# Kernel optimization log

Hardware: AMD Instinct MI355X
Metric: run time of the kernel (lower is better)

## Reference

```python
import jax, jax.numpy as jnp
import numpy as np

D = 128
N_DATA = 100000
N_TASK = 20000
E = 1000000


def _conv_params(key, d):
    ks = jax.random.split(key, 9)
    s = 1.0 / np.sqrt(d)
    return dict(
        Wmn=jax.random.uniform(ks[0], (d, d), jnp.float32, -s, s),
        bmn=jnp.zeros((d,), jnp.float32),
        Wme=jax.random.uniform(ks[1], (d, 1), jnp.float32, -1.0, 1.0),
        bme=jnp.zeros((d,), jnp.float32),
        Wgn=jax.random.uniform(ks[2], (d, d), jnp.float32, -s, s),
        bgn=jnp.zeros((d,), jnp.float32),
        Wge=jax.random.uniform(ks[3], (d, 1), jnp.float32, -1.0, 1.0),
        bge=jnp.zeros((d,), jnp.float32),
        bias=jnp.zeros((d,), jnp.float32),  # HeteConvLayer bias, zeros-init
    )


def setup_inputs() -> dict:
    key = jax.random.key(0)
    ks = jax.random.split(key, 12)
    inp = {
        'x_data': jax.random.normal(ks[0], (N_DATA, D), jnp.float32),
        'x_task': jax.random.normal(ks[1], (N_TASK, D), jnp.float32),
        'src_dt': jax.random.randint(ks[2], (E,), 0, N_DATA, jnp.int32),
        'dst_dt': jax.random.randint(ks[3], (E,), 0, N_TASK, jnp.int32),
        'ef_dt': jax.random.uniform(ks[4], (E, 1), jnp.float32),
        'src_td': jax.random.randint(ks[5], (E,), 0, N_TASK, jnp.int32),
        'dst_td': jax.random.randint(ks[6], (E,), 0, N_DATA, jnp.int32),
        'ef_td': jax.random.uniform(ks[7], (E, 1), jnp.float32),
    }
    # two separate HeteConvLayers (cfg.kg.hete=True)
    for name, k in (('dt', ks[8]), ('td', ks[9])):
        for pn, pv in _conv_params(k, D).items():
            inp[pn + '_' + name] = pv
    s = 1.0 / np.sqrt(D)
    inp['Ws_data'] = jax.random.uniform(ks[10], (D, D), jnp.float32, -s, s)
    inp['bs_data'] = jnp.zeros((D,), jnp.float32)
    inp['Ws_task'] = jax.random.uniform(ks[11], (D, D), jnp.float32, -s, s)
    inp['bs_task'] = jnp.zeros((D,), jnp.float32)
    return inp


def _hete_conv(x_neigh, src, dst, ef, Wmn, bmn, Wme, bme, Wgn, bgn, Wge, bge, bias, n_out):
    xj = x_neigh[src]                                   # [E, D] gather
    msg = xj @ Wmn.T + bmn + ef @ Wme.T + bme           # [E, D]
    gate = jax.nn.sigmoid(xj @ Wgn.T + bgn + ef @ Wge.T + bge) - 0.5  # gate_bias
    msg = msg * gate
    return jax.ops.segment_sum(msg, dst, num_segments=n_out) + bias


def _self_layer(x, Ws, bs):
    return (jax.nn.sigmoid(x @ Ws.T + bs) + 0.5) * x    # SelfLayer, gate_bias=True


def reference(x_data, x_task, src_dt, dst_dt, ef_dt, src_td, dst_td, ef_td,
              Wmn_dt, bmn_dt, Wme_dt, bme_dt, Wgn_dt, bgn_dt, Wge_dt, bge_dt, bias_dt,
              Wmn_td, bmn_td, Wme_td, bme_td, Wgn_td, bgn_td, Wge_td, bge_td, bias_td,
              Ws_data, bs_data, Ws_task, bs_task):
    # message type (data, property, task): neigh=data, self=task
    agg_task = _hete_conv(x_data, src_dt, dst_dt, ef_dt,
                          Wmn_dt, bmn_dt, Wme_dt, bme_dt,
                          Wgn_dt, bgn_dt, Wge_dt, bge_dt, bias_dt, N_TASK)
    # message type (task, property, data): neigh=task, self=data
    agg_data = _hete_conv(x_task, src_td, dst_td, ef_td,
                          Wmn_td, bmn_td, Wme_td, bme_td,
                          Wgn_td, bgn_td, Wge_td, bge_td, bias_td, N_DATA)
    # add self-transform, aggr='add', then Postlayer = ReLU
    data_emb = jax.nn.relu(agg_data + _self_layer(x_data, Ws_data, bs_data))
    task_emb = jax.nn.relu(agg_task + _self_layer(x_task, Ws_task, bs_task))
    # concatenate node-type outputs along node axis for a single output array
    return jnp.concatenate([data_emb, task_emb], axis=0)
```

## Files before the change

kernel.cpp:

```cpp
#include <hip/hip_runtime.h>
#include <hip/hip_bf16.h>
#include <cstdint>
#include <cstddef>

#define D_DIM 128
#define NEG_LOG2E (-1.44269504f)

typedef __attribute__((ext_vector_type(8))) short short8;
typedef __attribute__((ext_vector_type(4))) float f32x4;

__device__ __forceinline__ float sigmoid_fast(float z) {
  return __builtin_amdgcn_rcpf(1.0f + __expf(-z));
}

__device__ __forceinline__ unsigned short f2bf(float f) {
  union { float f; unsigned u; } v; v.f = f;
  unsigned r = v.u + 0x7FFF + ((v.u >> 16) & 1);
  return (unsigned short)(r >> 16);
}
__device__ __forceinline__ float bf_lo(unsigned u) { return __uint_as_float(u << 16); }
__device__ __forceinline__ float bf_hi(unsigned u) { return __uint_as_float(u & 0xFFFF0000u); }

__global__ __launch_bounds__(256) void fused_pre_kernel(
    const float* __restrict__ s0, const float* __restrict__ s1, const float* __restrict__ s2,
    const float* __restrict__ s3, const float* __restrict__ s4, const float* __restrict__ s5,
    short* __restrict__ wdst,
    const int* __restrict__ dst_dt, const int* __restrict__ dst_td,
    int* __restrict__ ghist, int* __restrict__ done,
    int* __restrict__ bbase, int* __restrict__ bcur, int* __restrict__ offsets,
    int nbt, int NB, int E, int n_tot) {
  __shared__ int lh[768];
  __shared__ int sc[256];
  __shared__ int lastflag;
  int t = threadIdx.x;

  if (blockIdx.x < 96) {
    int idx = blockIdx.x * 256 + t;
    int mat = idx >> 12;
    int pos = (idx & 4095) * 4;
    const float* s = (mat == 0) ? s0 : (mat == 1) ? s1 : (mat == 2) ? s2
                   : (mat == 3) ? s3 : (mat == 4) ? s4 : s5;
    float4 f = *(const float4*)(s + pos);
    short4 o;
    o.x = (short)f2bf(f.x); o.y = (short)f2bf(f.y);
    o.z = (short)f2bf(f.z); o.w = (short)f2bf(f.w);
    *(short4*)(wdst + mat * 16384 + pos) = o;
  }

  lh[t] = 0; lh[t + 256] = 0; lh[t + 512] = 0;
  __syncthreads();
  int E4 = E >> 2;
  for (int i = blockIdx.x * 256 + t; i < E4; i += gridDim.x * 256) {
    int4 a = *(const int4*)(dst_dt + 4 * i);
    atomicAdd(&lh[a.x >> 6], 1); atomicAdd(&lh[a.y >> 6], 1);
    atomicAdd(&lh[a.z >> 6], 1); atomicAdd(&lh[a.w >> 6], 1);
    int4 b = *(const int4*)(dst_td + 4 * i);
    atomicAdd(&lh[nbt + (b.x >> 8)], 1); atomicAdd(&lh[nbt + (b.y >> 8)], 1);
    atomicAdd(&lh[nbt + (b.z >> 8)], 1); atomicAdd(&lh[nbt + (b.w >> 8)], 1);
  }
  if (blockIdx.x == 0 && t < (E & 3)) {
    int j = (E & ~3) + t;
    atomicAdd(&lh[dst_dt[j] >> 6], 1);
    atomicAdd(&lh[nbt + (dst_td[j] >> 8)], 1);
  }
  __syncthreads();
#pragma unroll
  for (int k = 0; k < 3; ++k) {
    int b = t + k * 256;
    int c = lh[b];
    if (b < NB && c) atomicAdd(&ghist[b], c);
  }
  __threadfence();
  __syncthreads();
  if (t == 0) {
    int prev = atomicAdd(done, 1);
    lastflag = (prev == (int)gridDim.x - 1);
  }
  __syncthreads();
  if (!lastflag) return;
  __threadfence();

  int i0 = t * 3;
  int c0 = (i0     < NB) ? atomicAdd(&ghist[i0],     0) : 0;
  int c1 = (i0 + 1 < NB) ? atomicAdd(&ghist[i0 + 1], 0) : 0;
  int c2 = (i0 + 2 < NB) ? atomicAdd(&ghist[i0 + 2], 0) : 0;
  int tot = c0 + c1 + c2;
  sc[t] = tot; __syncthreads();
  for (int s = 1; s < 256; s <<= 1) {
    int u = (t >= s) ? sc[t - s] : 0;
    __syncthreads(); sc[t] += u; __syncthreads();
  }
  int base = sc[t] - tot;
  if (i0     < NB) { bbase[i0]     = base;           bcur[i0]     = base; }
  if (i0 + 1 < NB) { bbase[i0 + 1] = base + c0;      bcur[i0 + 1] = base + c0; }
  if (i0 + 2 < NB) { bbase[i0 + 2] = base + c0 + c1; bcur[i0 + 2] = base + c0 + c1; }
  if (t == 255) { bbase[NB] = sc[255]; offsets[n_tot] = sc[255]; }
}

__global__ __launch_bounds__(256) void node_mfma_all(
    const float* __restrict__ x_data, const float* __restrict__ x_task,
    const short* __restrict__ Wb,
    const float* __restrict__ bmn_dt, const float* __restrict__ bme_dt,
    const float* __restrict__ bgn_dt, const float* __restrict__ bge_dt,
    const float* __restrict__ bmn_td, const float* __restrict__ bme_td,
    const float* __restrict__ bgn_td, const float* __restrict__ bge_td,
    const float* __restrict__ bs_data, const float* __restrict__ bs_task,
    const float* __restrict__ bias_dt, const float* __restrict__ bias_td,
    unsigned int* __restrict__ YG_dt, unsigned int* __restrict__ YG_td,
    float* __restrict__ out, int n_data, int n_task, int gd) {
  __shared__ unsigned sh[32][132];
  const bool is_data = (int)blockIdx.x < gd;
  const float* x; const short *Wmnb, *Wgnb, *Wsb;
  const float *bmn, *bme, *bgn, *bge, *bs, *bias_other;
  unsigned* YG; float* out_init; int n, bid;
  if (is_data) {
    x = x_data; Wmnb = Wb; Wgnb = Wb + 16384; Wsb = Wb + 32768;
    bmn = bmn_dt; bme = bme_dt; bgn = bgn_dt; bge = bge_dt;
    bs = bs_data; bias_other = bias_td;
    YG = YG_dt; out_init = out; n = n_data; bid = blockIdx.x;
  } else {
    x = x_task; Wmnb = Wb + 3 * 16384; Wgnb = Wb + 4 * 16384; Wsb = Wb + 5 * 16384;
    bmn = bmn_td; bme = bme_td; bgn = bgn_td; bge = bge_td;
    bs = bs_task; bias_other = bias_dt;
    YG = YG_td; out_init = out + (size_t)n_data * D_DIM; n = n_task; bid = blockIdx.x - gd;
  }
  const int t = threadIdx.x;
  const int wave = t >> 6, lane = t & 63;
  const int q = lane >> 4, l15 = lane & 15;
  const int ng = wave >> 1;
  const int h = (wave & 1) * 64;
  const int base_node = bid * 32;
  const int node_base = base_node + ng * 16;

  short8 a[4];
  {
    int m = node_base + l15;
    int mc = m < n ? m : (n - 1);
    const float* xrow = x + (size_t)mc * D_DIM;
#pragma unroll
    for (int ks = 0; ks < 4; ++ks) {
      float4 f0 = *(const float4*)(xrow + ks * 32 + q * 8);
      float4 f1 = *(const float4*)(xrow + ks * 32 + q * 8 + 4);
      union { short8 s; __hip_bfloat162 hh[4]; } u;
      u.hh[0] = __float22bfloat162_rn({f0.x, f0.y});
      u.hh[1] = __float22bfloat162_rn({f0.z, f0.w});
      u.hh[2] = __float22bfloat162_rn({f1.x, f1.y});
      u.hh[3] = __float22bfloat162_rn({f1.z, f1.w});
      a[ks] = u.s;
    }
  }

  f32x4 accY[4], accG[4], accS[4];
#pragma unroll
  for (int nt = 0; nt < 4; ++nt) { accY[nt] = {0,0,0,0}; accG[nt] = {0,0,0,0}; accS[nt] = {0,0,0,0}; }

#pragma unroll
  for (int nt = 0; nt < 4; ++nt) {
    const int row = h + nt * 16 + l15;
#pragma unroll
    for (int ks = 0; ks < 4; ++ks) {
      const int off = row * D_DIM + ks * 32 + q * 8;
      short8 bm  = *(const short8*)(Wmnb + off);
      short8 bg  = *(const short8*)(Wgnb + off);
      short8 bsw = *(const short8*)(Wsb + off);
      accY[nt] = __builtin_amdgcn_mfma_f32_16x16x32_bf16(a[ks], bm,  accY[nt], 0, 0, 0);
      accG[nt] = __builtin_amdgcn_mfma_f32_16x16x32_bf16(a[ks], bg,  accG[nt], 0, 0, 0);
      accS[nt] = __builtin_amdgcn_mfma_f32_16x16x32_bf16(a[ks], bsw, accS[nt], 0, 0, 0);
    }
  }

#pragma unroll
  for (int nt = 0; nt < 4; ++nt) {
    int d = h + nt * 16 + l15;
    float bmv = bmn[d] + bme[d];
    float bgv = bgn[d] + bge[d];
#pragma unroll
    for (int r = 0; r < 4; ++r) {
      union { __hip_bfloat162 hh; unsigned u; } pck;
      pck.hh = __float22bfloat162_rn({accY[nt][r] + bmv,
                                      (accG[nt][r] + bgv) * NEG_LOG2E});
      sh[ng * 16 + q * 4 + r][d] = pck.u;
    }
  }
  __syncthreads();
#pragma unroll
  for (int it = 0; it < 4; ++it) {
    int idx = (it * 256 + t) * 4;
    int nl = idx >> 7, dd = idx & 127;
    int node = base_node + nl;
    if (node < n)
      *(uint4*)(YG + (size_t)node * D_DIM + dd) = *(const uint4*)&sh[nl][dd];
  }
  __syncthreads();

  float* shf = (float*)sh;
#pragma unroll
  for (int nt = 0; nt < 4; ++nt) {
    int d = h + nt * 16 + l15;
    float bsv = bs[d];
#pragma unroll
    for (int r = 0; r < 4; ++r)
      shf[(ng * 16 + q * 4 + r) * 132 + d] = sigmoid_fast(accS[nt][r] + bsv) + 0.5f;
  }
  __syncthreads();
#pragma unroll
  for (int it = 0; it < 4; ++it) {
    int idx = (it * 256 + t) * 4;
    int nl = idx >> 7, dd = idx & 127;
    int node = base_node + nl;
    if (node < n) {
      float4 xv = *(const float4*)(x + (size_t)node * D_DIM + dd);
      float4 bo = *(const float4*)(bias_other + dd);
      const float* sp = &shf[nl * 132 + dd];
      float4 o;
      o.x = sp[0] * xv.x + bo.x;
      o.y = sp[1] * xv.y + bo.y;
      o.z = sp[2] * xv.z + bo.z;
      o.w = sp[3] * xv.w + bo.w;
      *(float4*)(out_init + (size_t)node * D_DIM + dd) = o;
    }
  }
}

__global__ __launch_bounds__(256) void sort_a_kernel(
    const int* __restrict__ src_dt, const int* __restrict__ dst_dt, const float* __restrict__ ef_dt,
    const int* __restrict__ src_td, const int* __restrict__ dst_td, const float* __restrict__ ef_td,
    int* __restrict__ bcur, int2* __restrict__ eA, int nbt, int NB, int E) {
  __shared__ int lh[768];
  __shared__ int lcur[768];
  int t = threadIdx.x;
  lh[t] = 0; lh[t + 256] = 0; lh[t + 512] = 0;
  __syncthreads();
  int e0 = blockIdx.x * 4096;
  int e1 = min(E, e0 + 4096);
  const bool full = (e1 - e0 == 4096);
  if (full) {
#pragma unroll
    for (int k = 0; k < 4; ++k) {
      int b4 = e0 + (k * 256 + t) * 4;
      int4 d = *(const int4*)(dst_dt + b4);
      atomicAdd(&lh[d.x >> 6], 1); atomicAdd(&lh[d.y >> 6], 1);
      atomicAdd(&lh[d.z >> 6], 1); atomicAdd(&lh[d.w >> 6], 1);
      int4 d2 = *(const int4*)(dst_td + b4);
      atomicAdd(&lh[nbt + (d2.x >> 8)], 1); atomicAdd(&lh[nbt + (d2.y >> 8)], 1);
      atomicAdd(&lh[nbt + (d2.z >> 8)], 1); atomicAdd(&lh[nbt + (d2.w >> 8)], 1);
    }
  } else {
    for (int i = e0 + t; i < e1; i += 256) {
      atomicAdd(&lh[dst_dt[i] >> 6], 1);
      atomicAdd(&lh[nbt + (dst_td[i] >> 8)], 1);
    }
  }
  __syncthreads();
#pragma unroll
  for (int k = 0; k < 3; ++k) {
    int b = t + k * 256;
    int c = lh[b];
    if (b < NB && c) lcur[b] = atomicAdd(&bcur[b], c);
  }
  __syncthreads();
#define PUT_DT(ss, dd, ff) do { \
    int pos = atomicAdd(&lcur[(dd) >> 6], 1); \
    eA[pos] = make_int2((ss), (int)((__float_as_uint(ff) & 0xFFFFFF00u) | (unsigned)((dd) & 63))); \
  } while (0)
#define PUT_TD(ss, dd, ff) do { \
    int pos = atomicAdd(&lcur[nbt + ((dd) >> 8)], 1); \
    eA[pos] = make_int2((ss), (int)((__float_as_uint(ff) & 0xFFFFFF00u) | (unsigned)((dd) & 255))); \
  } while (0)
  if (full) {
#pragma unroll
    for (int k = 0; k < 4; ++k) {
      int b4 = e0 + (k * 256 + t) * 4;
      int4 s = *(const int4*)(src_dt + b4);
      int4 d = *(const int4*)(dst_dt + b4);
      float4 f = *(const float4*)(ef_dt + b4);
      PUT_DT(s.x, d.x, f.x); PUT_DT(s.y, d.y, f.y);
      PUT_DT(s.z, d.z, f.z); PUT_DT(s.w, d.w, f.w);
      s = *(const int4*)(src_td + b4);
      d = *(const int4*)(dst_td + b4);
      f = *(const float4*)(ef_td + b4);
      PUT_TD(s.x, d.x, f.x); PUT_TD(s.y, d.y, f.y);
      PUT_TD(s.z, d.z, f.z); PUT_TD(s.w, d.w, f.w);
    }
  } else {
    for (int i = e0 + t; i < e1; i += 256) {
      PUT_DT(src_dt[i], dst_dt[i], ef_dt[i]);
      PUT_TD(src_td[i], dst_td[i], ef_td[i]);
    }
  }
#undef PUT_DT
#undef PUT_TD
}

__global__ __launch_bounds__(256) void sort_b_kernel(
    const int2* __restrict__ eA, const int* __restrict__ bbase,
    int* __restrict__ offsets, int2* __restrict__ eB,
    int nbt, int n_task, int n_tot) {
  __shared__ int lh[256], sc[256], lcur[256];
  int b = blockIdx.x, t = threadIdx.x;
  int base = bbase[b];
  int cnt = bbase[b + 1] - base;
  int c0, nloc;
  if (b < nbt) { c0 = b << 6; nloc = min(64, n_task - c0); }
  else { c0 = n_task + ((b - nbt) << 8); nloc = min(256, n_tot - c0); }
  lh[t] = 0; __syncthreads();
  for (int i = base + t; i < base + cnt; i += 256)
    atomicAdd(&lh[((unsigned)eA[i].y) & 255u], 1);
  __syncthreads();
  int v = lh[t];
  sc[t] = v; __syncthreads();
  for (int s = 1; s < 256; s <<= 1) {
    int u = (t >= s) ? sc[t - s] : 0;
    __syncthreads(); sc[t] += u; __syncthreads();
  }
  int ex = sc[t] - v;
  lcur[t] = base + ex;
  if (t < nloc) offsets[c0 + t] = base + ex;
  __syncthreads();
  for (int i = base + t; i < base + cnt; i += 256) {
    int2 e = eA[i];
    int pos = atomicAdd(&lcur[((unsigned)e.y) & 255u], 1);
    eB[pos] = e;
  }
}

__device__ __forceinline__ void gs(float2& acc, int2 e, uint2 yv,
                                   float2 wme, float2 wge2) {
  float f = __int_as_float(e.y & (int)0xFFFFFF00);
  float g0 = __builtin_amdgcn_rcpf(1.0f + __builtin_amdgcn_exp2f(fmaf(f, wge2.x, bf_hi(yv.x)))) - 0.5f;
  float g1 = __builtin_amdgcn_rcpf(1.0f + __builtin_amdgcn_exp2f(fmaf(f, wge2.y, bf_hi(yv.y)))) - 0.5f;
  acc.x = fmaf(fmaf(f, wme.x, bf_lo(yv.x)), g0, acc.x);
  acc.y = fmaf(fmaf(f, wme.y, bf_lo(yv.y)), g1, acc.y);
}

__global__ __launch_bounds__(256) void gather_kernel(
    const unsigned* __restrict__ YG_dt, const unsigned* __restrict__ YG_td,
    const int* __restrict__ offsets, const int2* __restrict__ edata,
    const float* __restrict__ Wme_dt, const float* __restrict__ Wge_dt,
    const float* __restrict__ Wme_td, const float* __restrict__ Wge_td,
    float* __restrict__ out, int n_task, int n_data) {
  int w = (int)((blockIdx.x * 256u + threadIdx.x) >> 6);
  int lane = threadIdx.x & 63;
  if (w >= n_task + n_data) return;
  bool is_dt = w < n_task;
  const unsigned* YG = is_dt ? YG_dt : YG_td;
  const float* Wme = is_dt ? Wme_dt : Wme_td;
  const float* Wge = is_dt ? Wge_dt : Wge_td;
  size_t orow = is_dt ? (size_t)(n_data + w) : (size_t)(w - n_task);
  int beg = __builtin_amdgcn_readfirstlane(offsets[w]);
  int end = __builtin_amdgcn_readfirstlane(offsets[w + 1]);
  float2 wme = *(const float2*)(Wme + 2 * lane);
  float2 wge = *(const float2*)(Wge + 2 * lane);
  float2 wge2 = {wge.x * NEG_LOG2E, wge.y * NEG_LOG2E};
  float* op = out + orow * D_DIM + 2 * lane;
  float2 acc0 = *(const float2*)op;
  float2 acc1 = {0.0f, 0.0f}, acc2 = {0.0f, 0.0f}, acc3 = {0.0f, 0.0f};
  int p = beg;
#define YGLD(e) (*(const uint2*)(YG + (size_t)(e).x * D_DIM + 2 * lane))
  if (p + 8 <= end) {
    int2 e0 = edata[p],     e1 = edata[p + 1], e2 = edata[p + 2], e3 = edata[p + 3];
    int2 e4 = edata[p + 4], e5 = edata[p + 5], e6 = edata[p + 6], e7 = edata[p + 7];
    uint2 y0 = YGLD(e0), y1 = YGLD(e1), y2 = YGLD(e2), y3 = YGLD(e3);
    uint2 y4 = YGLD(e4), y5 = YGLD(e5), y6 = YGLD(e6), y7 = YGLD(e7);
    p += 8;
    for (; p + 8 <= end; p += 8) {
      int2 f0 = edata[p],     f1 = edata[p + 1], f2 = edata[p + 2], f3 = edata[p + 3];
      int2 f4 = edata[p + 4], f5 = edata[p + 5], f6 = edata[p + 6], f7 = edata[p + 7];
      uint2 z0 = YGLD(f0), z1 = YGLD(f1), z2 = YGLD(f2), z3 = YGLD(f3);
      uint2 z4 = YGLD(f4), z5 = YGLD(f5), z6 = YGLD(f6), z7 = YGLD(f7);
      gs(acc0, e0, y0, wme, wge2); gs(acc1, e1, y1, wme, wge2);
      gs(acc2, e2, y2, wme, wge2); gs(acc3, e3, y3, wme, wge2);
      gs(acc0, e4, y4, wme, wge2); gs(acc1, e5, y5, wme, wge2);
      gs(acc2, e6, y6, wme, wge2); gs(acc3, e7, y7, wme, wge2);
      e0 = f0; e1 = f1; e2 = f2; e3 = f3; e4 = f4; e5 = f5; e6 = f6; e7 = f7;
      y0 = z0; y1 = z1; y2 = z2; y3 = z3; y4 = z4; y5 = z5; y6 = z6; y7 = z7;
    }
    gs(acc0, e0, y0, wme, wge2); gs(acc1, e1, y1, wme, wge2);
    gs(acc2, e2, y2, wme, wge2); gs(acc3, e3, y3, wme, wge2);
    gs(acc0, e4, y4, wme, wge2); gs(acc1, e5, y5, wme, wge2);
    gs(acc2, e6, y6, wme, wge2); gs(acc3, e7, y7, wme, wge2);
  }
  for (; p < end; ++p) {
    int2 et = edata[p];
    uint2 yt = YGLD(et);
    gs(acc0, et, yt, wme, wge2);
  }
#undef YGLD
  acc0.x = fmaxf(acc0.x + acc1.x + acc2.x + acc3.x, 0.0f);
  acc0.y = fmaxf(acc0.y + acc1.y + acc2.y + acc3.y, 0.0f);
  *(float2*)op = acc0;
}

extern "C" void kernel_launch(void* const* d_in, const int* in_sizes, int n_in,
                              void* d_out, int out_size, void* d_ws, size_t ws_size,
                              hipStream_t stream) {
  const float* x_data  = (const float*)d_in[0];
  const float* x_task  = (const float*)d_in[1];
  const int*   src_dt  = (const int*)d_in[2];
  const int*   dst_dt  = (const int*)d_in[3];
  const float* ef_dt   = (const float*)d_in[4];
  const int*   src_td  = (const int*)d_in[5];
  const int*   dst_td  = (const int*)d_in[6];
  const float* ef_td   = (const float*)d_in[7];
  const float* Wmn_dt  = (const float*)d_in[8];
  const float* bmn_dt  = (const float*)d_in[9];
  const float* Wme_dt  = (const float*)d_in[10];
  const float* bme_dt  = (const float*)d_in[11];
  const float* Wgn_dt  = (const float*)d_in[12];
  const float* bgn_dt  = (const float*)d_in[13];
  const float* Wge_dt  = (const float*)d_in[14];
  const float* bge_dt  = (const float*)d_in[15];
  const float* bias_dt = (const float*)d_in[16];
  const float* Wmn_td  = (const float*)d_in[17];
  const float* bmn_td  = (const float*)d_in[18];
  const float* Wme_td  = (const float*)d_in[19];
  const float* bme_td  = (const float*)d_in[20];
  const float* Wgn_td  = (const float*)d_in[21];
  const float* bgn_td  = (const float*)d_in[22];
  const float* Wge_td  = (const float*)d_in[23];
  const float* bge_td  = (const float*)d_in[24];
  const float* bias_td = (const float*)d_in[25];
  const float* Ws_data = (const float*)d_in[26];
  const float* bs_data = (const float*)d_in[27];
  const float* Ws_task = (const float*)d_in[28];
  const float* bs_task = (const float*)d_in[29];
  float* out = (float*)d_out;

  const int N_DATA = in_sizes[0] / D_DIM;
  const int N_TASK = in_sizes[1] / D_DIM;
  const int E = in_sizes[2];
  const int N_TOT = N_TASK + N_DATA;
  const int NBT = (N_TASK + 63) >> 6;
  const int NBD = (N_DATA + 255) >> 8;
  const int NB = NBT + NBD;
  const int GD = (N_DATA + 31) / 32;
  const int GT = (N_TASK + 31) / 32;

  char* ws = (char*)d_ws;
  size_t off = 0;
  auto alloc = [&](size_t bytes) { void* p = ws + off; off += (bytes + 255) & ~(size_t)255; return p; };
  unsigned int* YG_dt = (unsigned int*)alloc((size_t)N_DATA * D_DIM * 4);
  unsigned int* YG_td = (unsigned int*)alloc((size_t)N_TASK * D_DIM * 4);
  int2* eA     = (int2*)alloc((size_t)2 * E * 8);
  int2* eB     = (int2*)alloc((size_t)2 * E * 8);
  int*  offs   = (int*)alloc((size_t)(N_TOT + 1) * 4);
  int*  ghist  = (int*)alloc(1024 * 4);
  int*  bbase  = (int*)alloc(768 * 4);
  int*  bcur   = (int*)alloc(768 * 4);
  short* Wb    = (short*)alloc((size_t)6 * 16384 * 2);
  (void)ws_size; (void)n_in; (void)out_size;

  hipMemsetAsync(ghist, 0, 1024 * 4, stream);

  fused_pre_kernel<<<256, 256, 0, stream>>>(
      Wmn_dt, Wgn_dt, Ws_data, Wmn_td, Wgn_td, Ws_task, Wb,
      dst_dt, dst_td, ghist, ghist + 768, bbase, bcur, offs,
      NBT, NB, E, N_TOT);

  node_mfma_all<<<GD + GT, 256, 0, stream>>>(
      x_data, x_task, Wb,
      bmn_dt, bme_dt, bgn_dt, bge_dt,
      bmn_td, bme_td, bgn_td, bge_td,
      bs_data, bs_task, bias_dt, bias_td,
      YG_dt, YG_td, out, N_DATA, N_TASK, GD);

  sort_a_kernel<<<(E + 4095) / 4096, 256, 0, stream>>>(
      src_dt, dst_dt, ef_dt, src_td, dst_td, ef_td, bcur, eA, NBT, NB, E);
  sort_b_kernel<<<NB, 256, 0, stream>>>(eA, bbase, offs, eB, NBT, N_TASK, N_TOT);

  gather_kernel<<<(N_TOT + 3) / 4, 256, 0, stream>>>(
      YG_dt, YG_td, offs, eB, Wme_dt, Wge_dt, Wme_td, Wge_td, out, N_TASK, N_DATA);
}
```

Baseline: 477.1 us.

## Split gather into per-relation launches, pre-scale source indices, drop software pipelining

```diff
diff --git a/kernel.cpp b/kernel.cpp
--- a/kernel.cpp
+++ b/kernel.cpp
@@ -320,7 +320,7 @@
   for (int i = base + t; i < base + cnt; i += 256) {
     int2 e = eA[i];
     int pos = atomicAdd(&lcur[((unsigned)e.y) & 255u], 1);
-    eB[pos] = e;
+    eB[pos] = make_int2(e.x << 7, e.y);
   }
 }
 
@@ -333,61 +333,47 @@
   acc.y = fmaf(fmaf(f, wme.y, bf_lo(yv.y)), g1, acc.y);
 }
 
-__global__ __launch_bounds__(256) void gather_kernel(
-    const unsigned* __restrict__ YG_dt, const unsigned* __restrict__ YG_td,
+__global__ __launch_bounds__(256) void gather_one_kernel(
+    const unsigned* __restrict__ YG,
     const int* __restrict__ offsets, const int2* __restrict__ edata,
-    const float* __restrict__ Wme_dt, const float* __restrict__ Wge_dt,
-    const float* __restrict__ Wme_td, const float* __restrict__ Wge_td,
-    float* __restrict__ out, int n_task, int n_data) {
+    const float* __restrict__ Wme, const float* __restrict__ Wge,
+    float* __restrict__ outp, int n) {
   int w = (int)((blockIdx.x * 256u + threadIdx.x) >> 6);
   int lane = threadIdx.x & 63;
-  if (w >= n_task + n_data) return;
-  bool is_dt = w < n_task;
-  const unsigned* YG = is_dt ? YG_dt : YG_td;
-  const float* Wme = is_dt ? Wme_dt : Wme_td;
-  const float* Wge = is_dt ? Wge_dt : Wge_td;
-  size_t orow = is_dt ? (size_t)(n_data + w) : (size_t)(w - n_task);
+  if (w >= n) return;
   int beg = __builtin_amdgcn_readfirstlane(offsets[w]);
   int end = __builtin_amdgcn_readfirstlane(offsets[w + 1]);
   float2 wme = *(const float2*)(Wme + 2 * lane);
   float2 wge = *(const float2*)(Wge + 2 * lane);
   float2 wge2 = {wge.x * NEG_LOG2E, wge.y * NEG_LOG2E};
-  float* op = out + orow * D_DIM + 2 * lane;
+  const unsigned* YGl = YG + 2 * lane;
+  float* op = outp + (size_t)w * D_DIM + 2 * lane;
   float2 acc0 = *(const float2*)op;
-  float2 acc1 = {0.0f, 0.0f}, acc2 = {0.0f, 0.0f}, acc3 = {0.0f, 0.0f};
+  float2 acc1 = {0.0f, 0.0f};
   int p = beg;
-#define YGLD(e) (*(const uint2*)(YG + (size_t)(e).x * D_DIM + 2 * lane))
-  if (p + 8 <= end) {
+  for (; p + 8 <= end; p += 8) {
     int2 e0 = edata[p],     e1 = edata[p + 1], e2 = edata[p + 2], e3 = edata[p + 3];
     int2 e4 = edata[p + 4], e5 = edata[p + 5], e6 = edata[p + 6], e7 = edata[p + 7];
-    uint2 y0 = YGLD(e0), y1 = YGLD(e1), y2 = YGLD(e2), y3 = YGLD(e3);
-    uint2 y4 = YGLD(e4), y5 = YGLD(e5), y6 = YGLD(e6), y7 = YGLD(e7);
-    p += 8;
-    for (; p + 8 <= end; p += 8) {
-      int2 f0 = edata[p],     f1 = edata[p + 1], f2 = edata[p + 2], f3 = edata[p + 3];
-      int2 f4 = edata[p + 4], f5 = edata[p + 5], f6 = edata[p + 6], f7 = edata[p + 7];
-      uint2 z0 = YGLD(f0), z1 = YGLD(f1), z2 = YGLD(f2), z3 = YGLD(f3);
-      uint2 z4 = YGLD(f4), z5 = YGLD(f5), z6 = YGLD(f6), z7 = YGLD(f7);
-      gs(acc0, e0, y0, wme, wge2); gs(acc1, e1, y1, wme, wge2);
-      gs(acc2, e2, y2, wme, wge2); gs(acc3, e3, y3, wme, wge2);
-      gs(acc0, e4, y4, wme, wge2); gs(acc1, e5, y5, wme, wge2);
-      gs(acc2, e6, y6, wme, wge2); gs(acc3, e7, y7, wme, wge2);
-      e0 = f0; e1 = f1; e2 = f2; e3 = f3; e4 = f4; e5 = f5; e6 = f6; e7 = f7;
-      y0 = z0; y1 = z1; y2 = z2; y3 = z3; y4 = z4; y5 = z5; y6 = z6; y7 = z7;
-    }
-    gs(acc0, e0, y0, wme, wge2); gs(acc1, e1, y1, wme, wge2);
-    gs(acc2, e2, y2, wme, wge2); gs(acc3, e3, y3, wme, wge2);
-    gs(acc0, e4, y4, wme, wge2); gs(acc1, e5, y5, wme, wge2);
-    gs(acc2, e6, y6, wme, wge2); gs(acc3, e7, y7, wme, wge2);
-  }
-  for (; p < end; ++p) {
-    int2 et = edata[p];
-    uint2 yt = YGLD(et);
-    gs(acc0, et, yt, wme, wge2);
-  }
-#undef YGLD
-  acc0.x = fmaxf(acc0.x + acc1.x + acc2.x + acc3.x, 0.0f);
-  acc0.y = fmaxf(acc0.y + acc1.y + acc2.y + acc3.y, 0.0f);
+    gs(acc0, e0, *(const uint2*)(YGl + e0.x), wme, wge2);
+    gs(acc1, e1, *(const uint2*)(YGl + e1.x), wme, wge2);
+    gs(acc0, e2, *(const uint2*)(YGl + e2.x), wme, wge2);
+    gs(acc1, e3, *(const uint2*)(YGl + e3.x), wme, wge2);
+    gs(acc0, e4, *(const uint2*)(YGl + e4.x), wme, wge2);
+    gs(acc1, e5, *(const uint2*)(YGl + e5.x), wme, wge2);
+    gs(acc0, e6, *(const uint2*)(YGl + e6.x), wme, wge2);
+    gs(acc1, e7, *(const uint2*)(YGl + e7.x), wme, wge2);
+  }
+  for (; p + 2 <= end; p += 2) {
+    int2 e0 = edata[p], e1 = edata[p + 1];
+    gs(acc0, e0, *(const uint2*)(YGl + e0.x), wme, wge2);
+    gs(acc1, e1, *(const uint2*)(YGl + e1.x), wme, wge2);
+  }
+  if (p < end) {
+    int2 e0 = edata[p];
+    gs(acc0, e0, *(const uint2*)(YGl + e0.x), wme, wge2);
+  }
+  acc0.x = fmaxf(acc0.x + acc1.x, 0.0f);
+  acc0.y = fmaxf(acc0.y + acc1.y, 0.0f);
   *(float2*)op = acc0;
 }
 
@@ -468,6 +454,8 @@
       src_dt, dst_dt, ef_dt, src_td, dst_td, ef_td, bcur, eA, NBT, NB, E);
   sort_b_kernel<<<NB, 256, 0, stream>>>(eA, bbase, offs, eB, NBT, N_TASK, N_TOT);
 
-  gather_kernel<<<(N_TOT + 3) / 4, 256, 0, stream>>>(
-      YG_dt, YG_td, offs, eB, Wme_dt, Wge_dt, Wme_td, Wge_td, out, N_TASK, N_DATA);
-}
+  gather_one_kernel<<<(N_TASK + 3) / 4, 256, 0, stream>>>(
+      YG_dt, offs, eB, Wme_dt, Wge_dt, out + (size_t)N_DATA * D_DIM, N_TASK);
+  gather_one_kernel<<<(N_DATA + 3) / 4, 256, 0, stream>>>(
+      YG_td, offs + N_TASK, eB, Wme_td, Wge_td, out, N_DATA);
+}
```

Result: no change. 475.2 us (-0.4%).
